# Kernel tuning notes

Measured on AMD Instinct MI355X. Metric: run time of the kernel, lower is better.

## Reference

```python
import jax, jax.numpy as jnp
import numpy as np

B, T, H, NIN, NOUT = 16, 64, 256, 2, 2
ALPHA = 0.25       # alpha_time_scale
BETA = 0.1         # beta_time_scale
SIGMA_SYN = 0.002
PERT_SIGMA = 0.1   # neural-noise sigma used only at t == perturbed_time


def setup_inputs() -> dict:
    key = jax.random.key(0)
    ks = jax.random.split(key, 8)
    return {
        'input_signal': jax.random.normal(ks[0], (B, T, NIN), jnp.float32),
        'hidden': jax.random.normal(ks[1], (B, H), jnp.float32) * 0.1,
        'w_in': jax.random.normal(ks[2], (H, NIN), jnp.float32) / np.sqrt(NIN).astype(np.float32),
        'w_hh': jax.random.normal(ks[3], (H, H), jnp.float32) / np.sqrt(H).astype(np.float32),
        'b_hh': jnp.zeros((H,), jnp.float32),
        'w_out': jax.random.normal(ks[4], (NOUT, H), jnp.float32) / np.sqrt(H).astype(np.float32),
        'noise_pert': jax.random.normal(ks[5], (B, H), jnp.float32),
        'syn_noise': jax.random.normal(ks[6], (T, B, H, H), jnp.float32),
        'perturbed_time': 32,
    }


def reference(input_signal, hidden, w_in, w_hh, b_hh, w_out, noise_pert, syn_noise, perturbed_time):
    # input_signal: [B,T,NIN]; hidden: [B,H]; plasticity (beta != 0) + anti-Hebbian branch.
    dt = input_signal.dtype
    Bn, Tn, _ = input_signal.shape
    Hn = hidden.shape[1]
    alpha = jnp.full((Hn,), ALPHA, dt)            # broadcasts over last (hidden) axis
    beta = jnp.full((Hn,), BETA, dt)
    sqrt_alpha = jnp.sqrt(alpha)
    sqrt_beta = jnp.sqrt(beta)

    xs_in = jnp.moveaxis(input_signal, 1, 0)      # [T,B,NIN]
    # new_j starts at w_hh; different_j = new_j - w_hh == 0, so it is derived each step.
    new_j0 = jnp.broadcast_to(w_hh, (Bn, Hn, Hn)).astype(dt)

    def step(carry, xs):
        h, new_j = carry
        x_t, sn_t, t = xs
        act = jnp.tanh(h)                                      # [B,H]
        diff_j = new_j - w_hh                                  # [B,H,H]
        # torch.matmul(act.unsqueeze(1), different_j).squeeze(1)
        dj_act = jnp.einsum('bi,bij->bj', act, diff_j)
        tmp = x_t @ w_in.T + act @ w_hh.T + b_hh + dj_act      # [B,H]
        noise = jnp.where(t == perturbed_time,
                          noise_pert * PERT_SIGMA * sqrt_alpha,
                          jnp.zeros((), dt))
        h = (1.0 - alpha) * h + alpha * tmp + noise
        # anti-Hebbian: -outer(act, act) + randn * sigma_syn * sqrt(beta)
        add_w = -jnp.einsum('bi,bj->bij', act, act) + sn_t * SIGMA_SYN * sqrt_beta
        new_j = new_j + beta * add_w                           # beta broadcasts on last axis
        out = h @ w_out.T                                      # [B,NOUT]
        return (h, new_j), (h, out)

    (h_fin, new_j), (hid_list, out_list) = jax.lax.scan(
        step, (hidden, new_j0), (xs_in, syn_noise, jnp.arange(Tn)))
    # [T,B,*] -> [B,T,*], matching the final permute in torch
    return (jnp.moveaxis(hid_list, 0, 1), jnp.moveaxis(out_list, 0, 1), h_fin, new_j)
```

## Files before the change

### kernel.cpp

```cpp
#include <hip/hip_runtime.h>

#define BB 16
#define TT 64
#define HH 256
#define NSUB 16
#define NBLK (BB * NSUB)

#define OUT_OFF  (BB * TT * HH)
#define HFIN_OFF (OUT_OFF + BB * TT * 2)
#define NJ_OFF   (HFIN_OFF + BB * HH)

#define C_SN    6.324555320336759e-05f
#define C_NOISE 0.05f

typedef unsigned long long u64;
typedef unsigned int u32;

__device__ __forceinline__ void slot_put(u64* p, u64 v) {
    (void)__hip_atomic_exchange(p, v, __ATOMIC_RELAXED, __HIP_MEMORY_SCOPE_AGENT);
}
__device__ __forceinline__ u64 slot_get(u64* p) {
    return __hip_atomic_fetch_add(p, 0ull, __ATOMIC_RELAXED, __HIP_MEMORY_SCOPE_AGENT);
}
__device__ __forceinline__ u64 pack(u32 tag, float v) {
    return ((u64)tag << 32) | (u64)__float_as_uint(v);
}

__global__ __launch_bounds__(256) void rnn_all(
    const float* __restrict__ x,
    const float* __restrict__ h0,
    const float* __restrict__ w_in,
    const float* __restrict__ w_hh,
    const float* __restrict__ b_hh,
    const float* __restrict__ w_out,
    const float* __restrict__ nper,
    const float* __restrict__ sn,
    const int*   __restrict__ pt_ptr,
    float*       __restrict__ dout,
    u64*         __restrict__ ws)
{
    const int tid = threadIdx.x;
    const int bid = blockIdx.x;
    const int b   = bid >> 4;
    const int sub = bid & 15;
    const int j0  = sub * 16;
    const int q     = tid & 15;
    const int rbase = tid >> 4;
    const int jcol  = j0 + q;
    const int wv = tid >> 6, ln = tid & 63;

    __shared__ float s_actT[2][HH];
    __shared__ float s_h[2][HH];
    __shared__ float s_red[4][16];
    __shared__ float s_o[4][2];
    __shared__ float s_x[2 * TT];
    __shared__ float s_wt[16][HH];

    u64* slotb = ws + (size_t)b * (2 * NSUB * 16);
    const int pt = *pt_ptr;

    for (int idx = tid; idx < 16 * HH; idx += 256)
        s_wt[idx >> 8][idx & 255] = w_hh[(size_t)(j0 + (idx >> 8)) * HH + (idx & 255)];
    {
        const float hv = h0[b * HH + tid];
        s_h[0][tid] = hv;
        s_actT[0][(tid & 15) * 16 + (tid >> 4)] = tanhf(hv);
    }
    if (tid < 2 * TT) s_x[tid] = x[b * 2 * TT + tid];

    float wi0 = 0.f, wi1 = 0.f, bh = 0.f, npv = 0.f, hreg = 0.f;
    if (tid < 16) {
        wi0  = w_in[jcol * 2 + 0];
        wi1  = w_in[jcol * 2 + 1];
        bh   = b_hh[jcol];
        npv  = nper[b * HH + jcol] * C_NOISE;
        hreg = h0[b * HH + jcol];
    }
    const float wo0 = w_out[tid], wo1 = w_out[HH + tid];
    __syncthreads();

    float M[16];
    #pragma unroll
    for (int m = 0; m < 16; ++m) M[m] = s_wt[q][rbase + 16 * m];

    float sreg[16];
    {
        const float* snp = sn + ((size_t)b * HH + rbase) * HH + jcol;
        #pragma unroll
        for (int m = 0; m < 16; ++m) sreg[m] = snp[(size_t)(16 * m) * HH];
    }

    for (int t = 0; t < TT; ++t) {
        const int cur = t & 1, nxt = cur ^ 1;
        const u32 tagw = (u32)(t + 1);

        float a[16];
        #pragma unroll
        for (int mq = 0; mq < 4; ++mq) {
            float4 v = *(const float4*)&s_actT[cur][rbase * 16 + mq * 4];
            a[mq * 4 + 0] = v.x; a[mq * 4 + 1] = v.y;
            a[mq * 4 + 2] = v.z; a[mq * 4 + 3] = v.w;
        }
        float p = 0.f;
        #pragma unroll
        for (int m = 0; m < 16; ++m) p += a[m] * M[m];
        p += __shfl_xor(p, 16, 64);
        p += __shfl_xor(p, 32, 64);
        if (ln < 16) s_red[wv][ln] = p;
        __syncthreads();

        if (tid < 16) {
            const float dj = s_red[0][tid] + s_red[1][tid]
                           + s_red[2][tid] + s_red[3][tid];
            const float tmp = s_x[2 * t] * wi0 + s_x[2 * t + 1] * wi1 + bh + dj;
            hreg = 0.75f * hreg + 0.25f * tmp + ((t == pt) ? npv : 0.f);
            slot_put(slotb + (cur * NSUB + sub) * 16 + tid, pack(tagw, hreg));
            s_h[nxt][jcol] = hreg;
            s_actT[nxt][q * 16 + sub] = tanhf(hreg);
            dout[((size_t)b * TT + t) * HH + jcol] = hreg;
        }

        const float aj = s_actT[cur][q * 16 + sub];
        #pragma unroll
        for (int m = 0; m < 16; ++m)
            M[m] += C_SN * sreg[m] - 0.1f * a[m] * aj;
        if (t + 1 < TT) {
            const float* snp = sn + (((size_t)(t + 1) * BB + b) * HH + rbase) * HH + jcol;
            #pragma unroll
            for (int m = 0; m < 16; ++m) sreg[m] = snp[(size_t)(16 * m) * HH];
        }
        if (sub == 1) {
            const float hv = s_h[cur][tid];
            float p0 = hv * wo0, p1 = hv * wo1;
            #pragma unroll
            for (int off = 32; off; off >>= 1) {
                p0 += __shfl_down(p0, off, 64);
                p1 += __shfl_down(p1, off, 64);
            }
            if (ln == 0) { s_o[wv][0] = p0; s_o[wv][1] = p1; }
        }

        if (tid < 240) {
            int fs = tid >> 4; fs += (fs >= sub);
            const int fq = tid & 15;
            u64* sp = slotb + (cur * NSUB + fs) * 16 + fq;
            u64 v = slot_get(sp);
            while ((u32)(v >> 32) != tagw) {
                __builtin_amdgcn_s_sleep(1);
                v = slot_get(sp);
            }
            const float hr = __uint_as_float((u32)v);
            s_h[nxt][fs * 16 + fq] = hr;
            s_actT[nxt][fq * 16 + fs] = tanhf(hr);
        }
        __syncthreads();

        if (sub == 1 && tid == 0 && t > 0) {
            dout[OUT_OFF + ((size_t)b * TT + (t - 1)) * 2 + 0] =
                s_o[0][0] + s_o[1][0] + s_o[2][0] + s_o[3][0];
            dout[OUT_OFF + ((size_t)b * TT + (t - 1)) * 2 + 1] =
                s_o[0][1] + s_o[1][1] + s_o[2][1] + s_o[3][1];
        }
    }

    if (sub == 1) {
        const float hv = s_h[0][tid];
        float p0 = hv * wo0, p1 = hv * wo1;
        #pragma unroll
        for (int off = 32; off; off >>= 1) {
            p0 += __shfl_down(p0, off, 64);
            p1 += __shfl_down(p1, off, 64);
        }
        if (ln == 0) { s_o[wv][0] = p0; s_o[wv][1] = p1; }
        __syncthreads();
        if (tid == 0) {
            dout[OUT_OFF + ((size_t)b * TT + (TT - 1)) * 2 + 0] =
                s_o[0][0] + s_o[1][0] + s_o[2][0] + s_o[3][0];
            dout[OUT_OFF + ((size_t)b * TT + (TT - 1)) * 2 + 1] =
                s_o[0][1] + s_o[1][1] + s_o[2][1] + s_o[3][1];
        }
    }
    if (sub == 2) dout[HFIN_OFF + b * HH + tid] = s_h[0][tid];

    #pragma unroll
    for (int m = 0; m < 16; ++m) {
        const int i = rbase + 16 * m;
        dout[NJ_OFF + ((size_t)b * HH + i) * HH + jcol] =
            w_hh[(size_t)i * HH + jcol] + M[m] - s_wt[q][i];
    }
}

extern "C" void kernel_launch(void* const* d_in, const int* in_sizes, int n_in,
                              void* d_out, int out_size, void* d_ws, size_t ws_size,
                              hipStream_t stream) {
    (void)in_sizes; (void)n_in; (void)out_size; (void)ws_size;
    const float* x     = (const float*)d_in[0];
    const float* h0    = (const float*)d_in[1];
    const float* w_in  = (const float*)d_in[2];
    const float* w_hh  = (const float*)d_in[3];
    const float* b_hh  = (const float*)d_in[4];
    const float* w_out = (const float*)d_in[5];
    const float* nper  = (const float*)d_in[6];
    const float* sn    = (const float*)d_in[7];
    const int*   pt    = (const int*)d_in[8];
    float* dout        = (float*)d_out;
    u64* ws            = (u64*)d_ws;

    hipMemsetAsync(d_ws, 0, (size_t)BB * 2 * NSUB * 16 * sizeof(u64), stream);

    rnn_all<<<dim3(NBLK), dim3(256), 0, stream>>>(
        x, h0, w_in, w_hh, b_hh, w_out, nper, sn, pt, dout, ws);
}
```

Baseline: 135.6 us.

## Add workgroup-scope fast exchange path with agent-scope fallback and remap block indices

Each hidden-state value is now published twice: once with workgroup-scope atomics and once with agent-scope atomics. Consumers first spin on the workgroup-scope copy and switch permanently to the agent-scope slot if the tag does not arrive within a bounded number of tries. The block-to-(batch, slice) mapping is swapped so that blocks sharing a batch are spread across the grid rather than adjacent. The workgroup-scope path relies on the 16 blocks of a batch sharing a cache, which is not guaranteed across XCDs, so its benefit depends on placement, and it adds extra writes and possible fallback latency.

```diff
diff --git a/kernel.cpp b/kernel.cpp
--- a/kernel.cpp
+++ b/kernel.cpp
@@ -13,14 +13,22 @@
 #define C_SN    6.324555320336759e-05f
 #define C_NOISE 0.05f
 
+#define SLOTS_PER_B (2 * NSUB * 16)
+
 typedef unsigned long long u64;
 typedef unsigned int u32;
 
-__device__ __forceinline__ void slot_put(u64* p, u64 v) {
+__device__ __forceinline__ void ag_put(u64* p, u64 v) {
     (void)__hip_atomic_exchange(p, v, __ATOMIC_RELAXED, __HIP_MEMORY_SCOPE_AGENT);
 }
-__device__ __forceinline__ u64 slot_get(u64* p) {
+__device__ __forceinline__ u64 ag_get(u64* p) {
     return __hip_atomic_fetch_add(p, 0ull, __ATOMIC_RELAXED, __HIP_MEMORY_SCOPE_AGENT);
+}
+__device__ __forceinline__ void wg_put(u64* p, u64 v) {
+    (void)__hip_atomic_exchange(p, v, __ATOMIC_RELAXED, __HIP_MEMORY_SCOPE_WORKGROUP);
+}
+__device__ __forceinline__ u64 wg_get(u64* p) {
+    return __hip_atomic_fetch_add(p, 0ull, __ATOMIC_RELAXED, __HIP_MEMORY_SCOPE_WORKGROUP);
 }
 __device__ __forceinline__ u64 pack(u32 tag, float v) {
     return ((u64)tag << 32) | (u64)__float_as_uint(v);
@@ -41,8 +49,8 @@
 {
     const int tid = threadIdx.x;
     const int bid = blockIdx.x;
-    const int b   = bid >> 4;
-    const int sub = bid & 15;
+    const int b   = bid & 15;
+    const int sub = bid >> 4;
     const int j0  = sub * 16;
     const int q     = tid & 15;
     const int rbase = tid >> 4;
@@ -56,7 +64,8 @@
     __shared__ float s_x[2 * TT];
     __shared__ float s_wt[16][HH];
 
-    u64* slotb = ws + (size_t)b * (2 * NSUB * 16);
+    u64* fastb = ws + (size_t)b * SLOTS_PER_B;
+    u64* agb   = ws + (size_t)(BB + b) * SLOTS_PER_B;
     const int pt = *pt_ptr;
 
     for (int idx = tid; idx < 16 * HH; idx += 256)
@@ -90,6 +99,8 @@
         for (int m = 0; m < 16; ++m) sreg[m] = snp[(size_t)(16 * m) * HH];
     }
 
+    bool useins = false;
+
     for (int t = 0; t < TT; ++t) {
         const int cur = t & 1, nxt = cur ^ 1;
         const u32 tagw = (u32)(t + 1);
@@ -114,7 +125,10 @@
                            + s_red[2][tid] + s_red[3][tid];
             const float tmp = s_x[2 * t] * wi0 + s_x[2 * t + 1] * wi1 + bh + dj;
             hreg = 0.75f * hreg + 0.25f * tmp + ((t == pt) ? npv : 0.f);
-            slot_put(slotb + (cur * NSUB + sub) * 16 + tid, pack(tagw, hreg));
+            const u64 pk = pack(tagw, hreg);
+            const int sidx = (cur * NSUB + sub) * 16 + tid;
+            wg_put(fastb + sidx, pk);
+            ag_put(agb + sidx, pk);
             s_h[nxt][jcol] = hreg;
             s_actT[nxt][q * 16 + sub] = tanhf(hreg);
             dout[((size_t)b * TT + t) * HH + jcol] = hreg;
@@ -143,11 +157,22 @@
         if (tid < 240) {
             int fs = tid >> 4; fs += (fs >= sub);
             const int fq = tid & 15;
-            u64* sp = slotb + (cur * NSUB + fs) * 16 + fq;
-            u64 v = slot_get(sp);
-            while ((u32)(v >> 32) != tagw) {
-                __builtin_amdgcn_s_sleep(1);
-                v = slot_get(sp);
+            const int sidx = (cur * NSUB + fs) * 16 + fq;
+            u64 v;
+            if (!useins) {
+                u64* fp = fastb + sidx;
+                v = wg_get(fp);
+                int tries = 0;
+                while ((u32)(v >> 32) != tagw && ++tries < 32) v = wg_get(fp);
+                if ((u32)(v >> 32) != tagw) useins = true;
+            }
+            if (useins) {
+                u64* ap = agb + sidx;
+                v = ag_get(ap);
+                while ((u32)(v >> 32) != tagw) {
+                    __builtin_amdgcn_s_sleep(1);
+                    v = ag_get(ap);
+                }
             }
             const float hr = __uint_as_float((u32)v);
             s_h[nxt][fs * 16 + fq] = hr;
@@ -206,7 +231,7 @@
     float* dout        = (float*)d_out;
     u64* ws            = (u64*)d_ws;
 
-    hipMemsetAsync(d_ws, 0, (size_t)BB * 2 * NSUB * 16 * sizeof(u64), stream);
+    hipMemsetAsync(d_ws, 0, (size_t)2 * BB * SLOTS_PER_B * sizeof(u64), stream);
 
     rnn_all<<<dim3(NBLK), dim3(256), 0, stream>>>(
         x, h0, w_in, w_hh, b_hh, w_out, nper, sn, pt, dout, ws);
```

Measured after the change: 173.6 us. +28.0%, slower.

## Add producer wavefront to prefetch synaptic noise into shared memory

Applied to the files above, without the earlier changes.

Adds a fifth wavefront per block whose only job is to load the next timestep's syn_noise tile from global memory, using float4 loads, into a double-buffered shared-memory array. The four compute wavefronts then read the noise from LDS instead of issuing strided per-thread global loads. The __syncthreads calls are replaced by a barrier that waits only on lgkmcnt, so the noise loads can overlap the recurrent dependency chain. In exchange the block uses extra LDS and a larger block size, and correctness now depends on the hand-written barrier handling the vmem waits.

```diff
diff --git a/kernel.cpp b/kernel.cpp
--- a/kernel.cpp
+++ b/kernel.cpp
@@ -5,6 +5,7 @@
 #define HH 256
 #define NSUB 16
 #define NBLK (BB * NSUB)
+#define NTH 320
 
 #define OUT_OFF  (BB * TT * HH)
 #define HFIN_OFF (OUT_OFF + BB * TT * 2)
@@ -13,6 +14,8 @@
 #define C_SN    6.324555320336759e-05f
 #define C_NOISE 0.05f
 
+#define SNP 20
+
 typedef unsigned long long u64;
 typedef unsigned int u32;
 
@@ -26,7 +29,14 @@
     return ((u64)tag << 32) | (u64)__float_as_uint(v);
 }
 
-__global__ __launch_bounds__(256) void rnn_all(
+#define LGKM_BAR() do {                                          \
+    asm volatile("s_waitcnt lgkmcnt(0)" ::: "memory");           \
+    __builtin_amdgcn_sched_barrier(0);                           \
+    __builtin_amdgcn_s_barrier();                                \
+    __builtin_amdgcn_sched_barrier(0);                           \
+} while (0)
+
+__global__ __launch_bounds__(NTH) void rnn_all(
     const float* __restrict__ x,
     const float* __restrict__ h0,
     const float* __restrict__ w_in,
@@ -45,9 +55,12 @@
     const int sub = bid & 15;
     const int j0  = sub * 16;
     const int q     = tid & 15;
-    const int rbase = tid >> 4;
+    const int rbase = (tid >> 4) & 15;
     const int jcol  = j0 + q;
     const int wv = tid >> 6, ln = tid & 63;
+    const bool cmp = (tid < 256);
+    const int dl = tid & 63;
+    const int dro = dl >> 2, dco = 4 * (dl & 3);
 
     __shared__ float s_actT[2][HH];
     __shared__ float s_h[2][HH];
@@ -55,18 +68,26 @@
     __shared__ float s_o[4][2];
     __shared__ float s_x[2 * TT];
     __shared__ float s_wt[16][HH];
+    __shared__ float s_sn[2][HH][SNP];
 
     u64* slotb = ws + (size_t)b * (2 * NSUB * 16);
     const int pt = *pt_ptr;
 
-    for (int idx = tid; idx < 16 * HH; idx += 256)
-        s_wt[idx >> 8][idx & 255] = w_hh[(size_t)(j0 + (idx >> 8)) * HH + (idx & 255)];
-    {
+    if (cmp) {
+        for (int idx = tid; idx < 16 * HH; idx += 256)
+            s_wt[idx >> 8][idx & 255] = w_hh[(size_t)(j0 + (idx >> 8)) * HH + (idx & 255)];
         const float hv = h0[b * HH + tid];
         s_h[0][tid] = hv;
         s_actT[0][(tid & 15) * 16 + (tid >> 4)] = tanhf(hv);
-    }
-    if (tid < 2 * TT) s_x[tid] = x[b * 2 * TT + tid];
+        if (tid < 2 * TT) s_x[tid] = x[b * 2 * TT + tid];
+    } else {
+        const float* snt = sn + (size_t)b * (HH * HH) + j0;
+        #pragma unroll
+        for (int k = 0; k < 16; ++k) {
+            float4 v = *(const float4*)&snt[(size_t)(16 * k + dro) * HH + dco];
+            *(float4*)&s_sn[0][16 * k + dro][dco] = v;
+        }
+    }
 
     float wi0 = 0.f, wi1 = 0.f, bh = 0.f, npv = 0.f, hreg = 0.f;
     if (tid < 16) {
@@ -76,18 +97,14 @@
         npv  = nper[b * HH + jcol] * C_NOISE;
         hreg = h0[b * HH + jcol];
     }
-    const float wo0 = w_out[tid], wo1 = w_out[HH + tid];
+    const float wo0 = cmp ? w_out[tid] : 0.f;
+    const float wo1 = cmp ? w_out[HH + tid] : 0.f;
     __syncthreads();
 
     float M[16];
-    #pragma unroll
-    for (int m = 0; m < 16; ++m) M[m] = s_wt[q][rbase + 16 * m];
-
-    float sreg[16];
-    {
-        const float* snp = sn + ((size_t)b * HH + rbase) * HH + jcol;
+    if (cmp) {
         #pragma unroll
-        for (int m = 0; m < 16; ++m) sreg[m] = snp[(size_t)(16 * m) * HH];
+        for (int m = 0; m < 16; ++m) M[m] = s_wt[q][rbase + 16 * m];
     }
 
     for (int t = 0; t < TT; ++t) {
@@ -95,65 +112,74 @@
         const u32 tagw = (u32)(t + 1);
 
         float a[16];
-        #pragma unroll
-        for (int mq = 0; mq < 4; ++mq) {
-            float4 v = *(const float4*)&s_actT[cur][rbase * 16 + mq * 4];
-            a[mq * 4 + 0] = v.x; a[mq * 4 + 1] = v.y;
-            a[mq * 4 + 2] = v.z; a[mq * 4 + 3] = v.w;
-        }
-        float p = 0.f;
-        #pragma unroll
-        for (int m = 0; m < 16; ++m) p += a[m] * M[m];
-        p += __shfl_xor(p, 16, 64);
-        p += __shfl_xor(p, 32, 64);
-        if (ln < 16) s_red[wv][ln] = p;
-        __syncthreads();
-
-        if (tid < 16) {
-            const float dj = s_red[0][tid] + s_red[1][tid]
-                           + s_red[2][tid] + s_red[3][tid];
-            const float tmp = s_x[2 * t] * wi0 + s_x[2 * t + 1] * wi1 + bh + dj;
-            hreg = 0.75f * hreg + 0.25f * tmp + ((t == pt) ? npv : 0.f);
-            slot_put(slotb + (cur * NSUB + sub) * 16 + tid, pack(tagw, hreg));
-            s_h[nxt][jcol] = hreg;
-            s_actT[nxt][q * 16 + sub] = tanhf(hreg);
-            dout[((size_t)b * TT + t) * HH + jcol] = hreg;
-        }
-
-        const float aj = s_actT[cur][q * 16 + sub];
-        #pragma unroll
-        for (int m = 0; m < 16; ++m)
-            M[m] += C_SN * sreg[m] - 0.1f * a[m] * aj;
-        if (t + 1 < TT) {
-            const float* snp = sn + (((size_t)(t + 1) * BB + b) * HH + rbase) * HH + jcol;
-            #pragma unroll
-            for (int m = 0; m < 16; ++m) sreg[m] = snp[(size_t)(16 * m) * HH];
-        }
-        if (sub == 1) {
-            const float hv = s_h[cur][tid];
-            float p0 = hv * wo0, p1 = hv * wo1;
-            #pragma unroll
-            for (int off = 32; off; off >>= 1) {
-                p0 += __shfl_down(p0, off, 64);
-                p1 += __shfl_down(p1, off, 64);
-            }
-            if (ln == 0) { s_o[wv][0] = p0; s_o[wv][1] = p1; }
-        }
-
-        if (tid < 240) {
-            int fs = tid >> 4; fs += (fs >= sub);
-            const int fq = tid & 15;
-            u64* sp = slotb + (cur * NSUB + fs) * 16 + fq;
-            u64 v = slot_get(sp);
-            while ((u32)(v >> 32) != tagw) {
-                __builtin_amdgcn_s_sleep(1);
-                v = slot_get(sp);
-            }
-            const float hr = __uint_as_float((u32)v);
-            s_h[nxt][fs * 16 + fq] = hr;
-            s_actT[nxt][fq * 16 + fs] = tanhf(hr);
-        }
-        __syncthreads();
+        float4 vs[16];
+        if (cmp) {
+            #pragma unroll
+            for (int mq = 0; mq < 4; ++mq) {
+                float4 v = *(const float4*)&s_actT[cur][rbase * 16 + mq * 4];
+                a[mq * 4 + 0] = v.x; a[mq * 4 + 1] = v.y;
+                a[mq * 4 + 2] = v.z; a[mq * 4 + 3] = v.w;
+            }
+            float p = 0.f;
+            #pragma unroll
+            for (int m = 0; m < 16; ++m) p += a[m] * M[m];
+            p += __shfl_xor(p, 16, 64);
+            p += __shfl_xor(p, 32, 64);
+            if (ln < 16) s_red[wv][ln] = p;
+        } else if (t + 1 < TT) {
+            const float* snt = sn + ((size_t)(t + 1) * BB + b) * (HH * HH) + j0;
+            #pragma unroll
+            for (int k = 0; k < 16; ++k)
+                vs[k] = *(const float4*)&snt[(size_t)(16 * k + dro) * HH + dco];
+        }
+        LGKM_BAR();
+
+        if (cmp) {
+            if (tid < 16) {
+                const float dj = s_red[0][tid] + s_red[1][tid]
+                               + s_red[2][tid] + s_red[3][tid];
+                const float tmp = s_x[2 * t] * wi0 + s_x[2 * t + 1] * wi1 + bh + dj;
+                hreg = 0.75f * hreg + 0.25f * tmp + ((t == pt) ? npv : 0.f);
+                slot_put(slotb + (cur * NSUB + sub) * 16 + tid, pack(tagw, hreg));
+                s_h[nxt][jcol] = hreg;
+                s_actT[nxt][q * 16 + sub] = tanhf(hreg);
+            }
+            {
+                const float aj = s_actT[cur][q * 16 + sub];
+                #pragma unroll
+                for (int m = 0; m < 16; ++m)
+                    M[m] += C_SN * s_sn[cur][rbase + 16 * m][q] - 0.1f * a[m] * aj;
+            }
+            if (sub == 1) {
+                const float hv = s_h[cur][tid];
+                float p0 = hv * wo0, p1 = hv * wo1;
+                #pragma unroll
+                for (int off = 32; off; off >>= 1) {
+                    p0 += __shfl_down(p0, off, 64);
+                    p1 += __shfl_down(p1, off, 64);
+                }
+                if (ln == 0) { s_o[wv][0] = p0; s_o[wv][1] = p1; }
+            }
+            if (tid < 240) {
+                int fs = tid >> 4; fs += (fs >= sub);
+                const int fq = tid & 15;
+                u64* sp = slotb + (cur * NSUB + fs) * 16 + fq;
+                u64 v = slot_get(sp);
+                while ((u32)(v >> 32) != tagw) {
+                    __builtin_amdgcn_s_sleep(1);
+                    v = slot_get(sp);
+                }
+                const float hr = __uint_as_float((u32)v);
+                s_h[nxt][fs * 16 + fq] = hr;
+                s_actT[nxt][fq * 16 + fs] = tanhf(hr);
+            }
+            if (tid < 16) dout[((size_t)b * TT + t) * HH + jcol] = hreg;
+        } else if (t + 1 < TT) {
+            #pragma unroll
+            for (int k = 0; k < 16; ++k)
+                *(float4*)&s_sn[nxt][16 * k + dro][dco] = vs[k];
+        }
+        LGKM_BAR();
 
         if (sub == 1 && tid == 0 && t > 0) {
             dout[OUT_OFF + ((size_t)b * TT + (t - 1)) * 2 + 0] =
@@ -164,14 +190,17 @@
     }
 
     if (sub == 1) {
-        const float hv = s_h[0][tid];
-        float p0 = hv * wo0, p1 = hv * wo1;
-        #pragma unroll
-        for (int off = 32; off; off >>= 1) {
-            p0 += __shfl_down(p0, off, 64);
-            p1 += __shfl_down(p1, off, 64);
-        }
-        if (ln == 0) { s_o[wv][0] = p0; s_o[wv][1] = p1; }
+        float p0 = 0.f, p1 = 0.f;
+        if (cmp) {
+            const float hv = s_h[0][tid];
+            p0 = hv * wo0; p1 = hv * wo1;
+            #pragma unroll
+            for (int off = 32; off; off >>= 1) {
+                p0 += __shfl_down(p0, off, 64);
+                p1 += __shfl_down(p1, off, 64);
+            }
+            if (ln == 0) { s_o[wv][0] = p0; s_o[wv][1] = p1; }
+        }
         __syncthreads();
         if (tid == 0) {
             dout[OUT_OFF + ((size_t)b * TT + (TT - 1)) * 2 + 0] =
@@ -180,13 +209,15 @@
                 s_o[0][1] + s_o[1][1] + s_o[2][1] + s_o[3][1];
         }
     }
-    if (sub == 2) dout[HFIN_OFF + b * HH + tid] = s_h[0][tid];
-
-    #pragma unroll
-    for (int m = 0; m < 16; ++m) {
-        const int i = rbase + 16 * m;
-        dout[NJ_OFF + ((size_t)b * HH + i) * HH + jcol] =
-            w_hh[(size_t)i * HH + jcol] + M[m] - s_wt[q][i];
+    if (sub == 2 && cmp) dout[HFIN_OFF + b * HH + tid] = s_h[0][tid];
+
+    if (cmp) {
+        #pragma unroll
+        for (int m = 0; m < 16; ++m) {
+            const int i = rbase + 16 * m;
+            dout[NJ_OFF + ((size_t)b * HH + i) * HH + jcol] =
+                w_hh[(size_t)i * HH + jcol] + M[m] - s_wt[q][i];
+        }
     }
 }
 
@@ -208,6 +239,6 @@
 
     hipMemsetAsync(d_ws, 0, (size_t)BB * 2 * NSUB * 16 * sizeof(u64), stream);
 
-    rnn_all<<<dim3(NBLK), dim3(256), 0, stream>>>(
+    rnn_all<<<dim3(NBLK), dim3(NTH), 0, stream>>>(
         x, h0, w_in, w_hh, b_hh, w_out, nper, sn, pt, dout, ws);
 }
```

Measured after the change: 180.1 us. 1.33x slower.
